# Kernel optimization log

Hardware: AMD Instinct MI355X
Metric: run time of the kernel (lower is better)

Reference implementation:

```python
import jax, jax.numpy as jnp
import numpy as np

VOCAB = 50257
DIM = 1024
B, S = 4, 4096


def setup_inputs() -> dict:
    key = jax.random.key(0)
    k1, k2, k3 = jax.random.split(key, 3)
    input_ids = jax.random.randint(k1, (B, S), 0, VOCAB)
    weight = jax.random.normal(k2, (VOCAB, DIM), dtype=jnp.float32)
    # R initialized as a random matrix stand-in for the learned Stiefel rotation
    R = jax.random.normal(k3, (DIM, DIM), dtype=jnp.float32) / np.sqrt(DIM)
    return {"input_ids": input_ids, "weight": weight, "R": R}


def reference(input_ids, weight, R):
    # Faithful to the module: rotate the FULL embedding table, then gather.
    w_eff = weight @ R              # [V, D] @ [D, D] -> [V, D]
    return jnp.take(w_eff, input_ids, axis=0)  # [B, S, D]
```

## Files before the change

kernel.cpp:

```cpp
#include <hip/hip_runtime.h>
#include <hip/hip_bf16.h>


typedef __attribute__((ext_vector_type(4))) float f32x4;
typedef __attribute__((ext_vector_type(8))) short s16x8;
typedef __attribute__((ext_vector_type(2))) int i32x2;

#define DIM 1024
#define NTK 32

__device__ __forceinline__ short f2bf(float f) {
  unsigned u = __float_as_uint(f);
  unsigned r = (u + 0x7FFFu + ((u >> 16) & 1u)) >> 16;
  return (short)r;
}

__device__ __forceinline__ void gload_lds16(const void* g, void* l) {
  __builtin_amdgcn_global_load_lds((const __attribute__((address_space(1))) void*)g,
                                   (__attribute__((address_space(3))) void*)l, 16, 0, 0);
}

__global__ __launch_bounds__(256) void prep_kernel(const float* __restrict__ R,
                                                   short* __restrict__ RT,
                                                   const float* __restrict__ W,
                                                   const int* __restrict__ ids,
                                                   short* __restrict__ G) {
  const int b = blockIdx.x;
  const int t = threadIdx.x;
  if (b < 1024) {
    __shared__ float tile[32][33];
    const int bx = b & 31, by = b >> 5;
    const int tx = t & 31, ty = t >> 5;
#pragma unroll
    for (int i = 0; i < 4; ++i)
      tile[ty + i * 8][tx] = R[(size_t)(by * 32 + ty + i * 8) * DIM + bx * 32 + tx];
    __syncthreads();
#pragma unroll
    for (int i = 0; i < 4; ++i)
      RT[(size_t)(bx * 32 + ty + i * 8) * DIM + by * 32 + tx] = f2bf(tile[tx][ty + i * 8]);
  } else {
    const int tid = (b - 1024) * 256 + t;
#pragma unroll
    for (int i = 0; i < 8; ++i) {
      const int g = tid + i * (2048 * 256);
      const int row = g >> 8;
      const int c4 = (g & 255) << 2;
      const f32x4 v = *(const f32x4*)(W + (size_t)ids[row] * DIM + c4);
      i32x2 p;
      p[0] = (int)(unsigned short)f2bf(v[0]) | ((int)f2bf(v[1]) << 16);
      p[1] = (int)(unsigned short)f2bf(v[2]) | ((int)f2bf(v[3]) << 16);
      *(i32x2*)(G + (size_t)g * 4) = p;
    }
  }
}

__global__ __launch_bounds__(256, 3) void rot_embed_gemm(const short* __restrict__ G,
                                                         const short* __restrict__ RT,
                                                         float* __restrict__ out) {
  extern __shared__ char smem[];

  const int t = threadIdx.x;
  const int b = blockIdx.x;
  const int swz = (b & 7) * 128 + (b >> 3);
  const int m0 = (swz >> 3) * 128;
  const int n0 = (swz & 7) * 128;

  const int lane = t & 63;
  const int w = t >> 6;
  const int wm = w >> 1, wn = w & 1;
  const int fr = lane & 15, fq = lane >> 4;

  char* const ldsA = smem;
  char* const ldsB = smem + 24576;

  const int scol = ((t & 3) ^ ((t >> 2) & 3) ^ ((t >> 4) & 3)) * 8;
  const short* gA = G + (size_t)(m0 + (t >> 2)) * DIM + scol;
  const short* gB = RT + (size_t)(n0 + (t >> 2)) * DIM + scol;
  const int dOff = w * 1024;

#define STG(buf, kt)                                                       \
  {                                                                        \
    gload_lds16(gA + (kt) * 32, ldsA + (buf) * 8192 + dOff);               \
    gload_lds16(gA + (size_t)64 * DIM + (kt) * 32,                         \
                ldsA + (buf) * 8192 + 4096 + dOff);                        \
    gload_lds16(gB + (kt) * 32, ldsB + (buf) * 8192 + dOff);               \
    gload_lds16(gB + (size_t)64 * DIM + (kt) * 32,                         \
                ldsB + (buf) * 8192 + 4096 + dOff);                        \
  }

  f32x4 acc[4][4];
#pragma unroll
  for (int i = 0; i < 4; ++i)
#pragma unroll
    for (int j = 0; j < 4; ++j) acc[i][j] = (f32x4)0.0f;

  const int sl = ((fq ^ (fr & 3) ^ ((fr >> 2) & 3)) & 3) << 4;

  STG(0, 0);
  STG(1, 1);

  for (int kt = 0; kt < NTK; ++kt) {
    if (kt == NTK - 1)
      asm volatile("s_waitcnt vmcnt(0)" ::: "memory");
    else
      asm volatile("s_waitcnt vmcnt(4)" ::: "memory");
    asm volatile("s_waitcnt lgkmcnt(0)" ::: "memory");
    __builtin_amdgcn_s_barrier();

    if (kt + 2 < NTK) STG((kt + 2) % 3, kt + 2);

    const char* A = ldsA + (kt % 3) * 8192;
    const char* B = ldsB + (kt % 3) * 8192;
    s16x8 af[4], bfv[4];
#pragma unroll
    for (int i = 0; i < 4; ++i) {
      af[i] = *(const s16x8*)(A + (wm * 64 + i * 16 + fr) * 64 + sl);
      bfv[i] = *(const s16x8*)(B + (wn * 64 + i * 16 + fr) * 64 + sl);
    }
    __builtin_amdgcn_s_setprio(1);
#pragma unroll
    for (int mi = 0; mi < 4; ++mi)
#pragma unroll
      for (int nj = 0; nj < 4; ++nj)
        acc[mi][nj] = __builtin_amdgcn_mfma_f32_16x16x32_bf16(af[mi], bfv[nj], acc[mi][nj], 0, 0, 0);
    __builtin_amdgcn_s_setprio(0);
  }

#pragma unroll
  for (int mi = 0; mi < 4; ++mi)
#pragma unroll
    for (int nj = 0; nj < 4; ++nj) {
      float* op = out + (size_t)(m0 + wm * 64 + mi * 16 + fq * 4) * DIM +
                  (n0 + wn * 64 + nj * 16 + fr);
#pragma unroll
      for (int r = 0; r < 4; ++r)
        __builtin_nontemporal_store(acc[mi][nj][r], op + (size_t)r * DIM);
    }
#undef STG
}

extern "C" void kernel_launch(void* const* d_in, const int* in_sizes, int n_in,
                              void* d_out, int out_size, void* d_ws, size_t ws_size,
                              hipStream_t stream) {
  const int* ids = (const int*)d_in[0];
  const float* W = (const float*)d_in[1];
  const float* R = (const float*)d_in[2];
  float* out = (float*)d_out;
  short* RT = (short*)d_ws;
  short* G = (short*)d_ws + (size_t)DIM * DIM;

  prep_kernel<<<dim3(3072), dim3(256), 0, stream>>>(R, RT, W, ids, G);
  rot_embed_gemm<<<dim3(1024), dim3(256), 49152, stream>>>(G, RT, out);
}
```

Measured before the change: 66.67 us.

## Enlarge GEMM tile to 256x128 with double-buffered LDS pipeline

Doubles the M dimension of each block tile to 256 rows, so each warp computes 128x64 and the grid halves to 512 blocks. The aim is to raise arithmetic intensity and reuse of the B tile. The triple-buffered prefetch-two pipeline is replaced by a double buffer with a full wait and barrier at the end of every iteration. That exposes more load latency and halves occupancy to 2 blocks per CU, and with 512 blocks on the MI355X's CUs there may be fewer waves to hide latency.

```diff
diff --git a/kernel.cpp b/kernel.cpp
--- a/kernel.cpp
+++ b/kernel.cpp
@@ -54,15 +54,15 @@
   }
 }
 
-__global__ __launch_bounds__(256, 3) void rot_embed_gemm(const short* __restrict__ G,
+__global__ __launch_bounds__(256, 2) void rot_embed_gemm(const short* __restrict__ G,
                                                          const short* __restrict__ RT,
                                                          float* __restrict__ out) {
   extern __shared__ char smem[];
 
   const int t = threadIdx.x;
   const int b = blockIdx.x;
-  const int swz = (b & 7) * 128 + (b >> 3);
-  const int m0 = (swz >> 3) * 128;
+  const int swz = (b & 7) * 64 + (b >> 3);
+  const int m0 = (swz >> 3) * 256;
   const int n0 = (swz & 7) * 128;
 
   const int lane = t & 63;
@@ -71,66 +71,65 @@
   const int fr = lane & 15, fq = lane >> 4;
 
   char* const ldsA = smem;
-  char* const ldsB = smem + 24576;
+  char* const ldsB = smem + 32768;
 
   const int scol = ((t & 3) ^ ((t >> 2) & 3) ^ ((t >> 4) & 3)) * 8;
   const short* gA = G + (size_t)(m0 + (t >> 2)) * DIM + scol;
   const short* gB = RT + (size_t)(n0 + (t >> 2)) * DIM + scol;
   const int dOff = w * 1024;
 
-#define STG(buf, kt)                                                       \
-  {                                                                        \
-    gload_lds16(gA + (kt) * 32, ldsA + (buf) * 8192 + dOff);               \
-    gload_lds16(gA + (size_t)64 * DIM + (kt) * 32,                         \
-                ldsA + (buf) * 8192 + 4096 + dOff);                        \
-    gload_lds16(gB + (kt) * 32, ldsB + (buf) * 8192 + dOff);               \
-    gload_lds16(gB + (size_t)64 * DIM + (kt) * 32,                         \
-                ldsB + (buf) * 8192 + 4096 + dOff);                        \
+#define STG(buf, kt)                                                        \
+  {                                                                         \
+    _Pragma("unroll") for (int j = 0; j < 4; ++j)                           \
+        gload_lds16(gA + (size_t)(j * 64) * DIM + (kt) * 32,                \
+                    ldsA + (buf) * 16384 + j * 4096 + dOff);                \
+    _Pragma("unroll") for (int j = 0; j < 2; ++j)                           \
+        gload_lds16(gB + (size_t)(j * 64) * DIM + (kt) * 32,                \
+                    ldsB + (buf) * 8192 + j * 4096 + dOff);                 \
   }
 
-  f32x4 acc[4][4];
+  f32x4 acc[8][4];
 #pragma unroll
-  for (int i = 0; i < 4; ++i)
+  for (int i = 0; i < 8; ++i)
 #pragma unroll
     for (int j = 0; j < 4; ++j) acc[i][j] = (f32x4)0.0f;
 
-  const int sl = ((fq ^ (fr & 3) ^ ((fr >> 2) & 3)) & 3) << 4;
+  const int sl = (fq ^ (fr & 3) ^ ((fr >> 2) & 3)) << 4;
 
   STG(0, 0);
-  STG(1, 1);
+  asm volatile("s_waitcnt vmcnt(0)" ::: "memory");
+  __builtin_amdgcn_s_barrier();
 
   for (int kt = 0; kt < NTK; ++kt) {
-    if (kt == NTK - 1)
-      asm volatile("s_waitcnt vmcnt(0)" ::: "memory");
-    else
-      asm volatile("s_waitcnt vmcnt(4)" ::: "memory");
-    asm volatile("s_waitcnt lgkmcnt(0)" ::: "memory");
-    __builtin_amdgcn_s_barrier();
+    const int buf = kt & 1;
+    if (kt + 1 < NTK) STG(buf ^ 1, kt + 1);
 
-    if (kt + 2 < NTK) STG((kt + 2) % 3, kt + 2);
-
-    const char* A = ldsA + (kt % 3) * 8192;
-    const char* B = ldsB + (kt % 3) * 8192;
-    s16x8 af[4], bfv[4];
+    const char* A = ldsA + buf * 16384;
+    const char* B = ldsB + buf * 8192;
+    s16x8 af[8], bfv[4];
 #pragma unroll
-    for (int i = 0; i < 4; ++i) {
-      af[i] = *(const s16x8*)(A + (wm * 64 + i * 16 + fr) * 64 + sl);
+    for (int i = 0; i < 8; ++i)
+      af[i] = *(const s16x8*)(A + (wm * 128 + i * 16 + fr) * 64 + sl);
+#pragma unroll
+    for (int i = 0; i < 4; ++i)
       bfv[i] = *(const s16x8*)(B + (wn * 64 + i * 16 + fr) * 64 + sl);
-    }
     __builtin_amdgcn_s_setprio(1);
 #pragma unroll
-    for (int mi = 0; mi < 4; ++mi)
+    for (int mi = 0; mi < 8; ++mi)
 #pragma unroll
       for (int nj = 0; nj < 4; ++nj)
         acc[mi][nj] = __builtin_amdgcn_mfma_f32_16x16x32_bf16(af[mi], bfv[nj], acc[mi][nj], 0, 0, 0);
     __builtin_amdgcn_s_setprio(0);
+
+    asm volatile("s_waitcnt vmcnt(0) lgkmcnt(0)" ::: "memory");
+    __builtin_amdgcn_s_barrier();
   }
 
 #pragma unroll
-  for (int mi = 0; mi < 4; ++mi)
+  for (int mi = 0; mi < 8; ++mi)
 #pragma unroll
     for (int nj = 0; nj < 4; ++nj) {
-      float* op = out + (size_t)(m0 + wm * 64 + mi * 16 + fq * 4) * DIM +
+      float* op = out + (size_t)(m0 + wm * 128 + mi * 16 + fq * 4) * DIM +
                   (n0 + wn * 64 + nj * 16 + fr);
 #pragma unroll
       for (int r = 0; r < 4; ++r)
@@ -150,5 +149,5 @@
   short* G = (short*)d_ws + (size_t)DIM * DIM;
 
   prep_kernel<<<dim3(3072), dim3(256), 0, stream>>>(R, RT, W, ids, G);
-  rot_embed_gemm<<<dim3(1024), dim3(256), 49152, stream>>>(G, RT, out);
+  rot_embed_gemm<<<dim3(512), dim3(256), 49152, stream>>>(G, RT, out);
 }
```

After: 67.49 us. About the same (+1.2%).
